# Kernel tuning notes

Measured on AMD Instinct MI355X. Metric: run time of the kernel, lower is better.

## Reference

```python
import jax, jax.numpy as jnp
import numpy as np

N = 50000        # nodes
E = 800000       # edges (avg degree 16)
B = 128          # graphs in batch
NODE_F, EDGE_F, GLOB_F = 16, 8, 32
H = 64           # hidden_dim
L = 4            # num_layers
C = 9            # threshold classes
NG, GE = 20, 16  # num gate types, gate embedding dim
MSG_IN = H + EDGE_F + GE   # 88
UPD_IN = 2 * H             # 128


def _ln(x, g, b):
    mu = x.mean(-1, keepdims=True)
    v = ((x - mu) ** 2).mean(-1, keepdims=True)
    return (x - mu) / jnp.sqrt(v + 1e-5) * g + b


def setup_inputs() -> dict:
    key = jax.random.key(0)
    ks = jax.random.split(key, 24)
    w = lambda k, shp: (jax.random.normal(k, shp, jnp.float32) * 0.05)
    inp = {
        'x': jax.random.normal(ks[0], (N, NODE_F), jnp.float32),
        'edge_index': jax.random.randint(ks[1], (2, E), 0, N, jnp.int32),
        'edge_attr': jax.random.normal(ks[2], (E, EDGE_F), jnp.float32),
        'edge_gate_type': jax.random.randint(ks[3], (E,), 0, NG, jnp.int32),
        'batch': jnp.sort(jax.random.randint(ks[4], (N,), 0, B, jnp.int32)),
        'global_features': jax.random.normal(ks[5], (B, GLOB_F), jnp.float32),
        # node_embed
        'W_embed': w(ks[6], (NODE_F, H)), 'b_embed': jnp.zeros((H,), jnp.float32),
        'g_eln': jnp.ones((H,), jnp.float32), 'b_eln': jnp.zeros((H,), jnp.float32),
        # message-passing layers (stacked over L)
        'mp_gate_emb': w(ks[7], (L, NG, GE)),
        'mp_W_msg': w(ks[8], (L, MSG_IN, H)), 'mp_b_msg': jnp.zeros((L, H), jnp.float32),
        'mp_W_upd': w(ks[9], (L, UPD_IN, H)), 'mp_b_upd': jnp.zeros((L, H), jnp.float32),
        # global_proj
        'W_gproj': w(ks[10], (GLOB_F, H)), 'b_gproj': jnp.zeros((H,), jnp.float32),
        'g_gln': jnp.ones((H,), jnp.float32), 'b_gln': jnp.zeros((H,), jnp.float32),
        # combined_mlp
        'W_c1': w(ks[11], (3 * H + H, 2 * H)), 'b_c1': jnp.zeros((2 * H,), jnp.float32),
        'g_cln': jnp.ones((2 * H,), jnp.float32), 'b_cln': jnp.zeros((2 * H,), jnp.float32),
        'W_c2': w(ks[12], (2 * H, H)), 'b_c2': jnp.zeros((H,), jnp.float32),
        # head
        'W_head': w(ks[13], (H, C)), 'b_head': jnp.zeros((C,), jnp.float32),
    }
    return inp


def reference(x, edge_index, edge_attr, edge_gate_type, batch, global_features,
              W_embed, b_embed, g_eln, b_eln,
              mp_gate_emb, mp_W_msg, mp_b_msg, mp_W_upd, mp_b_upd,
              W_gproj, b_gproj, g_gln, b_gln,
              W_c1, b_c1, g_cln, b_cln, W_c2, b_c2, W_head, b_head):
    n_nodes = x.shape[0]
    n_graphs = global_features.shape[0]
    # node embed (dropout = identity in eval)
    h = _ln(jax.nn.relu(x @ W_embed + b_embed), g_eln, b_eln)  # [N,H]
    src, dst = edge_index[0], edge_index[1]
    for l in range(mp_W_msg.shape[0]):
        ge = mp_gate_emb[l][edge_gate_type]                     # [E,GE] gather
        m_in = jnp.concatenate([h[src], edge_attr, ge], axis=-1)  # [E,MSG_IN]
        m = jax.nn.relu(m_in @ mp_W_msg[l] + mp_b_msg[l])          # [E,H]
        agg = jax.ops.segment_sum(m, dst, num_segments=n_nodes)   # [N,H] scatter-add
        h_new = jnp.concatenate([h, agg], axis=-1) @ mp_W_upd[l] + mp_b_upd[l]
        h = h + h_new                                              # residual
    # multi global pooling
    ones = jnp.ones((n_nodes,), h.dtype)
    counts = jax.ops.segment_sum(ones, batch, num_segments=n_graphs)[:, None]
    h_sum = jax.ops.segment_sum(h, batch, num_segments=n_graphs)
    h_mean = h_sum / jnp.maximum(counts, 1.0)
    h_max = jax.ops.segment_max(h, batch, num_segments=n_graphs)
    h_max = jnp.where(counts > 0, h_max, 0.0)
    h_graph = jnp.concatenate([h_mean, h_max, h_sum], axis=-1)   # [B,3H]
    g = _ln(jax.nn.relu(global_features @ W_gproj + b_gproj), g_gln, b_gln)
    c = jnp.concatenate([h_graph, g], axis=-1)                   # [B,4H]
    c = jax.nn.relu(c @ W_c1 + b_c1)
    c = _ln(c, g_cln, b_cln)
    c = jax.nn.relu(c @ W_c2 + b_c2)
    return c @ W_head + b_head                                   # [B,C]
```

## Files before the change

### kernel.cpp

```cpp
#include <hip/hip_runtime.h>

__device__ __forceinline__ int rfl(int v) { return __builtin_amdgcn_readfirstlane(v); }

__device__ __forceinline__ int lower_bound_dev(const int* __restrict__ a, int n, int v) {
  int lo = 0, hi = n;
  while (lo < hi) { int mid = (lo + hi) >> 1; if (a[mid] < v) lo = mid + 1; else hi = mid; }
  return lo;
}

__global__ void count_kernel(const int* __restrict__ dst, int* __restrict__ counts, int E) {
  int e = blockIdx.x * 256 + threadIdx.x;
  if (e < E) atomicAdd(&counts[dst[e]], 1);
}

__global__ __launch_bounds__(256) void scan_phase1(const int* __restrict__ counts,
                                                   int* __restrict__ row_ptr,
                                                   int* __restrict__ blocksums, int n) {
  int tid = threadIdx.x;
  int i0 = blockIdx.x * 1024 + tid * 4;
  int4 c = make_int4(0, 0, 0, 0);
  if (i0 + 3 < n) {
    c = *(const int4*)(counts + i0);
  } else {
    if (i0 + 0 < n) c.x = counts[i0 + 0];
    if (i0 + 1 < n) c.y = counts[i0 + 1];
    if (i0 + 2 < n) c.z = counts[i0 + 2];
    if (i0 + 3 < n) c.w = counts[i0 + 3];
  }
  int s = c.x + c.y + c.z + c.w;
  int lane = tid & 63, wave = tid >> 6;
  int v = s;
  for (int o = 1; o < 64; o <<= 1) { int u = __shfl_up(v, o); if (lane >= o) v += u; }
  __shared__ int wsum[4];
  if (lane == 63) wsum[wave] = v;
  __syncthreads();
  int woff = 0;
  for (int w = 0; w < wave; w++) woff += wsum[w];
  int excl = woff + (v - s);
  if (tid == 255) blocksums[blockIdx.x] = woff + v;
  int p0 = excl, p1 = p0 + c.x, p2 = p1 + c.y, p3 = p2 + c.z;
  if (i0 + 3 < n) {
    *(int4*)(row_ptr + i0) = make_int4(p0, p1, p2, p3);
  } else {
    if (i0 + 0 < n) row_ptr[i0 + 0] = p0;
    if (i0 + 1 < n) row_ptr[i0 + 1] = p1;
    if (i0 + 2 < n) row_ptr[i0 + 2] = p2;
    if (i0 + 3 < n) row_ptr[i0 + 3] = p3;
  }
}

__global__ __launch_bounds__(64) void scan_phase2(int* __restrict__ blocksums, int nb) {
  int carry = 0;
  for (int base = 0; base < nb; base += 64) {
    int i = base + (int)threadIdx.x;
    int v = (i < nb) ? blocksums[i] : 0;
    int inc = v;
    for (int o = 1; o < 64; o <<= 1) { int u = __shfl_up(inc, o); if ((int)threadIdx.x >= o) inc += u; }
    if (i < nb) blocksums[i] = carry + inc - v;
    carry += __shfl(inc, 63);
  }
}

__global__ __launch_bounds__(256) void scan_phase3(int* __restrict__ row_ptr,
                                                   const int* __restrict__ blocksums,
                                                   int* __restrict__ nextp, int n, int E) {
  int i = blockIdx.x * 256 + threadIdx.x;
  if (i < n) {
    int v = row_ptr[i] + blocksums[i >> 10];
    row_ptr[i] = v;
    nextp[i] = v;
  }
  if (i == 0) row_ptr[n] = E;
}

__global__ void scatter_kernel(const int* __restrict__ src, const int* __restrict__ dst,
                               const int* __restrict__ gt, const float* __restrict__ edge_attr,
                               int* __restrict__ nextp, int2* __restrict__ epk,
                               float* __restrict__ eap, int E) {
  int e = blockIdx.x * 256 + threadIdx.x;
  if (e < E) {
    int p = atomicAdd(&nextp[dst[e]], 1);
    epk[p] = make_int2(src[e], gt[e]);
    const float4* s = (const float4*)(edge_attr + (size_t)e * 8);
    float4 a0 = s[0], a1 = s[1];
    float4* d = (float4*)(eap + (size_t)p * 8);
    d[0] = a0; d[1] = a1;
  }
}

__global__ void gew_kernel(const float* __restrict__ gate_emb, const float* __restrict__ W_msg,
                           float* __restrict__ geW, int nrows) {
  int tid = threadIdx.x;
  int lane = tid & 63;
  int row = blockIdx.x * 4 + (tid >> 6);
  if (row >= nrows) return;
  int l = row / 20, t = row % 20;
  const float* ge = gate_emb + ((size_t)l * 20 + t) * 16;
  const float* W3 = W_msg + (size_t)l * 88 * 64 + 72 * 64;
  float acc = 0.f;
#pragma unroll
  for (int k = 0; k < 16; k++) acc = fmaf(ge[k], W3[(size_t)k * 64 + lane], acc);
  geW[(size_t)row * 64 + lane] = acc;
}

__global__ __launch_bounds__(256) void embed_kernel(const float* __restrict__ x,
                                                    const float* __restrict__ W,
                                                    const float* __restrict__ b,
                                                    const float* __restrict__ gamma,
                                                    const float* __restrict__ beta,
                                                    float* __restrict__ h, int n_nodes) {
  __shared__ float Ws[16 * 64];
  int tid = threadIdx.x;
  for (int i = tid; i < 16 * 64; i += 256) Ws[i] = W[i];
  __syncthreads();
  int lane = tid & 63;
  int n = blockIdx.x * 4 + (tid >> 6);
  if (n >= n_nodes) return;
  const float* xr = x + (size_t)n * 16;
  float acc = b[lane];
#pragma unroll
  for (int k = 0; k < 16; k++) acc = fmaf(xr[k], Ws[k * 64 + lane], acc);
  acc = fmaxf(acc, 0.f);
  float s = acc;
  for (int o = 32; o; o >>= 1) s += __shfl_xor(s, o);
  float mu = s * (1.f / 64.f);
  float d = acc - mu;
  float v = d * d;
  for (int o = 32; o; o >>= 1) v += __shfl_xor(v, o);
  float r = rsqrtf(v * (1.f / 64.f) + 1e-5f);
  h[(size_t)n * 64 + lane] = d * r * gamma[lane] + beta[lane];
}

__global__ __launch_bounds__(256) void nodelin_kernel(const float* __restrict__ A,
                                                      const float* __restrict__ W,
                                                      float* __restrict__ C, int n_nodes) {
  __shared__ float As[64 * 64];
  __shared__ float Bs[64 * 64];
  int tid = threadIdx.x;
  int n0 = blockIdx.x * 64;
#pragma unroll
  for (int i = 0; i < 4; i++) {
    int flat = (tid + i * 256) * 4;
    int r = flat >> 6, k = flat & 63;
    float4 f = make_float4(0.f, 0.f, 0.f, 0.f);
    int n = n0 + r;
    if (n < n_nodes) f = *(const float4*)(A + (size_t)n * 64 + k);
    As[(k + 0) * 64 + r] = f.x;
    As[(k + 1) * 64 + r] = f.y;
    As[(k + 2) * 64 + r] = f.z;
    As[(k + 3) * 64 + r] = f.w;
  }
#pragma unroll
  for (int i = 0; i < 4; i++) {
    int flat = (tid + i * 256) * 4;
    *(float4*)&Bs[flat] = *(const float4*)&W[flat];
  }
  __syncthreads();
  int tx = tid & 15, ty = tid >> 4;
  float acc[4][4] = {{0.f}};
#pragma unroll 4
  for (int k = 0; k < 64; k++) {
    float4 a = *(const float4*)&As[k * 64 + ty * 4];
    float4 bb = *(const float4*)&Bs[k * 64 + tx * 4];
    float av[4] = {a.x, a.y, a.z, a.w};
    float bv[4] = {bb.x, bb.y, bb.z, bb.w};
#pragma unroll
    for (int i = 0; i < 4; i++)
#pragma unroll
      for (int j = 0; j < 4; j++) acc[i][j] = fmaf(av[i], bv[j], acc[i][j]);
  }
#pragma unroll
  for (int i = 0; i < 4; i++) {
    int n = n0 + ty * 4 + i;
    if (n < n_nodes) {
      float4 o = make_float4(acc[i][0], acc[i][1], acc[i][2], acc[i][3]);
      *(float4*)&C[(size_t)n * 64 + tx * 4] = o;
    }
  }
}

__global__ __launch_bounds__(256) void edge_kernel(const float* __restrict__ hW,
                                                   const int2* __restrict__ epk,
                                                   const float* __restrict__ eap,
                                                   const int* __restrict__ row_ptr,
                                                   const float* __restrict__ W_msg_l,
                                                   const float* __restrict__ b_msg_l,
                                                   const float* __restrict__ geW_l,
                                                   float* __restrict__ agg, int n_nodes) {
  __shared__ float geWs[20 * 64];
  int tid = threadIdx.x;
  for (int i = tid; i < 20 * 64; i += 256) geWs[i] = geW_l[i];
  __syncthreads();
  int lane = tid & 63;
  int n = blockIdx.x * 4 + (tid >> 6);
  if (n >= n_nodes) return;
  float w2[8];
#pragma unroll
  for (int k = 0; k < 8; k++) w2[k] = W_msg_l[(size_t)(64 + k) * 64 + lane];
  float bm = b_msg_l[lane];
  int beg = rfl(row_ptr[n]);
  int end = rfl(row_ptr[n + 1]);
  float acc = 0.f;
  int idx = beg;
  for (; idx + 4 <= end; idx += 4) {
    int2 p0 = epk[idx + 0], p1 = epk[idx + 1], p2 = epk[idx + 2], p3 = epk[idx + 3];
    int s0 = rfl(p0.x), t0 = rfl(p0.y);
    int s1 = rfl(p1.x), t1 = rfl(p1.y);
    int s2 = rfl(p2.x), t2 = rfl(p2.y);
    int s3 = rfl(p3.x), t3 = rfl(p3.y);
    float g0 = hW[(size_t)s0 * 64 + lane];
    float g1 = hW[(size_t)s1 * 64 + lane];
    float g2 = hW[(size_t)s2 * 64 + lane];
    float g3 = hW[(size_t)s3 * 64 + lane];
    const float4* ep = (const float4*)(eap + (size_t)idx * 8);
    float4 a00 = ep[0], a01 = ep[1], a10 = ep[2], a11 = ep[3];
    float4 a20 = ep[4], a21 = ep[5], a30 = ep[6], a31 = ep[7];
    float v0 = g0 + geWs[t0 * 64 + lane] + bm;
    v0 = fmaf(a00.x, w2[0], v0); v0 = fmaf(a00.y, w2[1], v0);
    v0 = fmaf(a00.z, w2[2], v0); v0 = fmaf(a00.w, w2[3], v0);
    v0 = fmaf(a01.x, w2[4], v0); v0 = fmaf(a01.y, w2[5], v0);
    v0 = fmaf(a01.z, w2[6], v0); v0 = fmaf(a01.w, w2[7], v0);
    float v1 = g1 + geWs[t1 * 64 + lane] + bm;
    v1 = fmaf(a10.x, w2[0], v1); v1 = fmaf(a10.y, w2[1], v1);
    v1 = fmaf(a10.z, w2[2], v1); v1 = fmaf(a10.w, w2[3], v1);
    v1 = fmaf(a11.x, w2[4], v1); v1 = fmaf(a11.y, w2[5], v1);
    v1 = fmaf(a11.z, w2[6], v1); v1 = fmaf(a11.w, w2[7], v1);
    float v2 = g2 + geWs[t2 * 64 + lane] + bm;
    v2 = fmaf(a20.x, w2[0], v2); v2 = fmaf(a20.y, w2[1], v2);
    v2 = fmaf(a20.z, w2[2], v2); v2 = fmaf(a20.w, w2[3], v2);
    v2 = fmaf(a21.x, w2[4], v2); v2 = fmaf(a21.y, w2[5], v2);
    v2 = fmaf(a21.z, w2[6], v2); v2 = fmaf(a21.w, w2[7], v2);
    float v3 = g3 + geWs[t3 * 64 + lane] + bm;
    v3 = fmaf(a30.x, w2[0], v3); v3 = fmaf(a30.y, w2[1], v3);
    v3 = fmaf(a30.z, w2[2], v3); v3 = fmaf(a30.w, w2[3], v3);
    v3 = fmaf(a31.x, w2[4], v3); v3 = fmaf(a31.y, w2[5], v3);
    v3 = fmaf(a31.z, w2[6], v3); v3 = fmaf(a31.w, w2[7], v3);
    acc += fmaxf(v0, 0.f) + fmaxf(v1, 0.f) + fmaxf(v2, 0.f) + fmaxf(v3, 0.f);
  }
  for (; idx < end; idx++) {
    int2 p = epk[idx];
    int s = rfl(p.x), t = rfl(p.y);
    float g = hW[(size_t)s * 64 + lane];
    const float4* ep = (const float4*)(eap + (size_t)idx * 8);
    float4 a0 = ep[0], a1 = ep[1];
    float v = g + geWs[t * 64 + lane] + bm;
    v = fmaf(a0.x, w2[0], v); v = fmaf(a0.y, w2[1], v);
    v = fmaf(a0.z, w2[2], v); v = fmaf(a0.w, w2[3], v);
    v = fmaf(a1.x, w2[4], v); v = fmaf(a1.y, w2[5], v);
    v = fmaf(a1.z, w2[6], v); v = fmaf(a1.w, w2[7], v);
    acc += fmaxf(v, 0.f);
  }
  agg[(size_t)n * 64 + lane] = acc;
}

__global__ __launch_bounds__(256) void update_fused_kernel(const float* __restrict__ h,
                                                           const float* __restrict__ agg,
                                                           const float* __restrict__ Wu,
                                                           const float* __restrict__ bu,
                                                           const float* __restrict__ W1next,
                                                           float* __restrict__ h_out,
                                                           float* __restrict__ hW_out,
                                                           int n_nodes) {
  __shared__ float As[128 * 64];
  __shared__ float Bs[128 * 64];
  int tid = threadIdx.x;
  int n0 = blockIdx.x * 64;
#pragma unroll
  for (int i = 0; i < 8; i++) {
    int flat = (tid + i * 256) * 4;
    int r = flat >> 7, k = flat & 127;
    float4 f = make_float4(0.f, 0.f, 0.f, 0.f);
    int n = n0 + r;
    if (n < n_nodes) {
      const float* sp = (k < 64) ? (h + (size_t)n * 64 + k) : (agg + (size_t)n * 64 + (k - 64));
      f = *(const float4*)sp;
    }
    As[(k + 0) * 64 + r] = f.x;
    As[(k + 1) * 64 + r] = f.y;
    As[(k + 2) * 64 + r] = f.z;
    As[(k + 3) * 64 + r] = f.w;
  }
#pragma unroll
  for (int i = 0; i < 8; i++) {
    int flat = (tid + i * 256) * 4;
    *(float4*)&Bs[flat] = *(const float4*)&Wu[flat];
  }
  __syncthreads();
  int tx = tid & 15, ty = tid >> 4;
  float acc[4][4] = {{0.f}};
#pragma unroll 4
  for (int k = 0; k < 128; k++) {
    float4 a = *(const float4*)&As[k * 64 + ty * 4];
    float4 bb = *(const float4*)&Bs[k * 64 + tx * 4];
    float av[4] = {a.x, a.y, a.z, a.w};
    float bv[4] = {bb.x, bb.y, bb.z, bb.w};
#pragma unroll
    for (int i = 0; i < 4; i++)
#pragma unroll
      for (int j = 0; j < 4; j++) acc[i][j] = fmaf(av[i], bv[j], acc[i][j]);
  }
  float hnew[4][4];
  float4 bv4 = *(const float4*)&bu[tx * 4];
#pragma unroll
  for (int i = 0; i < 4; i++) {
    int n = n0 + ty * 4 + i;
    if (n < n_nodes) {
      float4 hv = *(const float4*)&h[(size_t)n * 64 + tx * 4];
      hnew[i][0] = hv.x + acc[i][0] + bv4.x;
      hnew[i][1] = hv.y + acc[i][1] + bv4.y;
      hnew[i][2] = hv.z + acc[i][2] + bv4.z;
      hnew[i][3] = hv.w + acc[i][3] + bv4.w;
      float4 o = make_float4(hnew[i][0], hnew[i][1], hnew[i][2], hnew[i][3]);
      *(float4*)&h_out[(size_t)n * 64 + tx * 4] = o;
    } else {
      hnew[i][0] = hnew[i][1] = hnew[i][2] = hnew[i][3] = 0.f;
    }
  }
  if (W1next) {
    __syncthreads();
#pragma unroll
    for (int i = 0; i < 4; i++)
#pragma unroll
      for (int j = 0; j < 4; j++) As[(tx * 4 + j) * 64 + (ty * 4 + i)] = hnew[i][j];
#pragma unroll
    for (int i = 0; i < 4; i++) {
      int flat = (tid + i * 256) * 4;
      *(float4*)&Bs[flat] = *(const float4*)&W1next[flat];
    }
    __syncthreads();
    float acc2[4][4] = {{0.f}};
#pragma unroll 4
    for (int k = 0; k < 64; k++) {
      float4 a = *(const float4*)&As[k * 64 + ty * 4];
      float4 bb = *(const float4*)&Bs[k * 64 + tx * 4];
      float av[4] = {a.x, a.y, a.z, a.w};
      float bv[4] = {bb.x, bb.y, bb.z, bb.w};
#pragma unroll
      for (int i = 0; i < 4; i++)
#pragma unroll
        for (int j = 0; j < 4; j++) acc2[i][j] = fmaf(av[i], bv[j], acc2[i][j]);
    }
#pragma unroll
    for (int i = 0; i < 4; i++) {
      int n = n0 + ty * 4 + i;
      if (n < n_nodes) {
        float4 o = make_float4(acc2[i][0], acc2[i][1], acc2[i][2], acc2[i][3]);
        *(float4*)&hW_out[(size_t)n * 64 + tx * 4] = o;
      }
    }
  }
}

__global__ __launch_bounds__(256) void pool_kernel(const float* __restrict__ h,
                                                   const int* __restrict__ batch,
                                                   float* __restrict__ pooled, int n_nodes) {
  int b = blockIdx.x;
  __shared__ int se[2];
  if (threadIdx.x == 0) se[0] = lower_bound_dev(batch, n_nodes, b);
  if (threadIdx.x == 1) se[1] = lower_bound_dev(batch, n_nodes, b + 1);
  __syncthreads();
  int start = se[0], end = se[1];
  int lane = threadIdx.x & 63, wave = threadIdx.x >> 6;
  float s = 0.f, m = -INFINITY;
  for (int i = start + wave; i < end; i += 4) {
    float v = h[(size_t)i * 64 + lane];
    s += v;
    m = fmaxf(m, v);
  }
  __shared__ float ss[4][64], mm[4][64];
  ss[wave][lane] = s;
  mm[wave][lane] = m;
  __syncthreads();
  if (wave == 0) {
    s = ss[0][lane] + ss[1][lane] + ss[2][lane] + ss[3][lane];
    m = fmaxf(fmaxf(mm[0][lane], mm[1][lane]), fmaxf(mm[2][lane], mm[3][lane]));
    int cnt = end - start;
    float mean = (cnt > 0) ? s / (float)cnt : 0.f;
    if (cnt == 0) { m = 0.f; s = 0.f; }
    pooled[(size_t)b * 192 + lane] = mean;
    pooled[(size_t)b * 192 + 64 + lane] = m;
    pooled[(size_t)b * 192 + 128 + lane] = s;
  }
}

__global__ __launch_bounds__(128) void mlp_kernel(
    const float* __restrict__ pooled, const float* __restrict__ glob,
    const float* __restrict__ W_gproj, const float* __restrict__ b_gproj,
    const float* __restrict__ g_gln, const float* __restrict__ b_gln,
    const float* __restrict__ W_c1, const float* __restrict__ b_c1,
    const float* __restrict__ g_cln, const float* __restrict__ b_cln,
    const float* __restrict__ W_c2, const float* __restrict__ b_c2,
    const float* __restrict__ W_head, const float* __restrict__ b_head,
    float* __restrict__ out) {
  int b = blockIdx.x;
  int tid = threadIdx.x;
  __shared__ float c[256];
  __shared__ float c1s[128];
  __shared__ float c2s[64];
  __shared__ float sred[2][2];
  c[tid] = pooled[(size_t)b * 192 + tid];
  if (tid < 64) c[128 + tid] = pooled[(size_t)b * 192 + 128 + tid];
  if (tid < 64) {
    const float* gf = glob + (size_t)b * 32;
    float acc = b_gproj[tid];
#pragma unroll
    for (int k = 0; k < 32; k++) acc = fmaf(gf[k], W_gproj[(size_t)k * 64 + tid], acc);
    acc = fmaxf(acc, 0.f);
    float s = acc;
    for (int o = 32; o; o >>= 1) s += __shfl_xor(s, o);
    float mu = s * (1.f / 64.f);
    float d = acc - mu;
    float v = d * d;
    for (int o = 32; o; o >>= 1) v += __shfl_xor(v, o);
    float r = rsqrtf(v * (1.f / 64.f) + 1e-5f);
    c[192 + tid] = d * r * g_gln[tid] + b_gln[tid];
  }
  __syncthreads();
  float acc = b_c1[tid];
  for (int k = 0; k < 256; k++) acc = fmaf(c[k], W_c1[(size_t)k * 128 + tid], acc);
  acc = fmaxf(acc, 0.f);
  float s = acc;
  for (int o = 32; o; o >>= 1) s += __shfl_xor(s, o);
  if ((tid & 63) == 0) sred[0][tid >> 6] = s;
  __syncthreads();
  float mu = (sred[0][0] + sred[0][1]) * (1.f / 128.f);
  float d = acc - mu;
  float v = d * d;
  for (int o = 32; o; o >>= 1) v += __shfl_xor(v, o);
  if ((tid & 63) == 0) sred[1][tid >> 6] = v;
  __syncthreads();
  float var = (sred[1][0] + sred[1][1]) * (1.f / 128.f);
  c1s[tid] = d * rsqrtf(var + 1e-5f) * g_cln[tid] + b_cln[tid];
  __syncthreads();
  if (tid < 64) {
    float a2 = b_c2[tid];
    for (int k = 0; k < 128; k++) a2 = fmaf(c1s[k], W_c2[(size_t)k * 64 + tid], a2);
    c2s[tid] = fmaxf(a2, 0.f);
  }
  __syncthreads();
  if (tid < 9) {
    float a3 = b_head[tid];
#pragma unroll
    for (int k = 0; k < 64; k++) a3 = fmaf(c2s[k], W_head[(size_t)k * 9 + tid], a3);
    out[(size_t)b * 9 + tid] = a3;
  }
}

extern "C" void kernel_launch(void* const* d_in, const int* in_sizes, int n_in,
                              void* d_out, int out_size, void* d_ws, size_t ws_size,
                              hipStream_t stream) {
  const float* x       = (const float*)d_in[0];
  const int* edge_index= (const int*)d_in[1];
  const float* edge_attr=(const float*)d_in[2];
  const int* gtype     = (const int*)d_in[3];
  const int* batch     = (const int*)d_in[4];
  const float* glob    = (const float*)d_in[5];
  const float* W_embed = (const float*)d_in[6];
  const float* b_embed = (const float*)d_in[7];
  const float* g_eln   = (const float*)d_in[8];
  const float* b_eln   = (const float*)d_in[9];
  const float* gate_emb= (const float*)d_in[10];
  const float* W_msg   = (const float*)d_in[11];
  const float* b_msg   = (const float*)d_in[12];
  const float* W_upd   = (const float*)d_in[13];
  const float* b_upd   = (const float*)d_in[14];
  const float* W_gproj = (const float*)d_in[15];
  const float* b_gproj = (const float*)d_in[16];
  const float* g_gln   = (const float*)d_in[17];
  const float* b_gln   = (const float*)d_in[18];
  const float* W_c1    = (const float*)d_in[19];
  const float* b_c1    = (const float*)d_in[20];
  const float* g_cln   = (const float*)d_in[21];
  const float* b_cln   = (const float*)d_in[22];
  const float* W_c2    = (const float*)d_in[23];
  const float* b_c2    = (const float*)d_in[24];
  const float* W_head  = (const float*)d_in[25];
  const float* b_head  = (const float*)d_in[26];

  const int N = in_sizes[0] / 16;
  const int E = in_sizes[1] / 2;
  const int B = in_sizes[5] / 32;
  const int L = in_sizes[12] / 64;

  const int* src = edge_index;
  const int* dst = edge_index + E;

  char* ws = (char*)d_ws;
  size_t off = 0;
  auto alloc = [&](size_t bytes) -> void* {
    void* p = ws + off;
    off += (bytes + 255) & ~(size_t)255;
    return p;
  };
  float* h      = (float*)alloc((size_t)N * 64 * 4);
  float* hW     = (float*)alloc((size_t)N * 64 * 4);
  float* agg    = (float*)alloc((size_t)N * 64 * 4);
  float* geW    = (float*)alloc((size_t)L * 20 * 64 * 4);
  float* pooled = (float*)alloc((size_t)B * 192 * 4);
  int* counts   = (int*)alloc((size_t)N * 4);
  int* row_ptr  = (int*)alloc((size_t)(N + 1) * 4);
  int* nextp    = (int*)alloc((size_t)N * 4);
  int nb = (N + 1023) / 1024;
  int* blocksums= (int*)alloc((size_t)nb * 4);
  int2* epk     = (int2*)alloc((size_t)E * 8);
  float* eap    = (float*)alloc((size_t)E * 8 * 4);

  hipMemsetAsync(counts, 0, (size_t)N * 4, stream);
  count_kernel<<<(E + 255) / 256, 256, 0, stream>>>(dst, counts, E);
  scan_phase1<<<nb, 256, 0, stream>>>(counts, row_ptr, blocksums, N);
  scan_phase2<<<1, 64, 0, stream>>>(blocksums, nb);
  scan_phase3<<<(N + 255) / 256, 256, 0, stream>>>(row_ptr, blocksums, nextp, N, E);
  scatter_kernel<<<(E + 255) / 256, 256, 0, stream>>>(src, dst, gtype, edge_attr,
                                                      nextp, epk, eap, E);
  gew_kernel<<<(L * 20 + 3) / 4, 256, 0, stream>>>(gate_emb, W_msg, geW, L * 20);
  embed_kernel<<<(N + 3) / 4, 256, 0, stream>>>(x, W_embed, b_embed, g_eln, b_eln, h, N);

  nodelin_kernel<<<(N + 63) / 64, 256, 0, stream>>>(h, W_msg, hW, N);
  for (int l = 0; l < L; l++) {
    edge_kernel<<<(N + 3) / 4, 256, 0, stream>>>(hW, epk, eap, row_ptr,
                                                 W_msg + (size_t)l * 88 * 64, b_msg + (size_t)l * 64,
                                                 geW + (size_t)l * 20 * 64, agg, N);
    const float* W1next = (l + 1 < L) ? (W_msg + (size_t)(l + 1) * 88 * 64) : nullptr;
    update_fused_kernel<<<(N + 63) / 64, 256, 0, stream>>>(h, agg, W_upd + (size_t)l * 128 * 64,
                                                           b_upd + (size_t)l * 64, W1next, h, hW, N);
  }

  pool_kernel<<<B, 256, 0, stream>>>(h, batch, pooled, N);
  mlp_kernel<<<B, 128, 0, stream>>>(pooled, glob, W_gproj, b_gproj, g_gln, b_gln,
                                    W_c1, b_c1, g_cln, b_cln, W_c2, b_c2,
                                    W_head, b_head, (float*)d_out);
}
```

Measured before the change: 517.4 us.

## Split CSR scatter into permutation plus gather, pack edge metadata, drop LDS staging

Edge sorting now runs in two steps. The first scatters only a permutation index via atomics, and the second gathers src, gate type and edge attributes with coalesced writes. Source and gate type are packed into one 32-bit word (20-bit src), which halves per-edge metadata reads in the edge kernel. The edge kernel also stops staging the gate-weight table in shared memory and reads it directly from global/L2, removing a block-wide barrier. Costs are an extra kernel launch and permutation buffer, plus an implicit limit of fewer than about one million nodes and at most 2047 gate types.

Result: no change. 516.2 us (-0.2%).

```diff
diff --git a/kernel.cpp b/kernel.cpp
--- a/kernel.cpp
+++ b/kernel.cpp
@@ -73,17 +73,22 @@
   if (i == 0) row_ptr[n] = E;
 }
 
-__global__ void scatter_kernel(const int* __restrict__ src, const int* __restrict__ dst,
-                               const int* __restrict__ gt, const float* __restrict__ edge_attr,
-                               int* __restrict__ nextp, int2* __restrict__ epk,
-                               float* __restrict__ eap, int E) {
+__global__ void scatter_perm(const int* __restrict__ dst, int* __restrict__ nextp,
+                             int* __restrict__ perm, int E) {
   int e = blockIdx.x * 256 + threadIdx.x;
-  if (e < E) {
-    int p = atomicAdd(&nextp[dst[e]], 1);
-    epk[p] = make_int2(src[e], gt[e]);
+  if (e < E) { int p = atomicAdd(&nextp[dst[e]], 1); perm[p] = e; }
+}
+
+__global__ void gather_build(const int* __restrict__ perm, const int* __restrict__ src,
+                             const int* __restrict__ gt, const float* __restrict__ edge_attr,
+                             int* __restrict__ epack, float* __restrict__ eap, int E) {
+  int idx = blockIdx.x * 256 + threadIdx.x;
+  if (idx < E) {
+    int e = perm[idx];
+    epack[idx] = (gt[e] << 20) | src[e];
     const float4* s = (const float4*)(edge_attr + (size_t)e * 8);
     float4 a0 = s[0], a1 = s[1];
-    float4* d = (float4*)(eap + (size_t)p * 8);
+    float4* d = (float4*)(eap + (size_t)idx * 8);
     d[0] = a0; d[1] = a1;
   }
 }
@@ -180,17 +185,14 @@
 }
 
 __global__ __launch_bounds__(256) void edge_kernel(const float* __restrict__ hW,
-                                                   const int2* __restrict__ epk,
+                                                   const int* __restrict__ epack,
                                                    const float* __restrict__ eap,
                                                    const int* __restrict__ row_ptr,
                                                    const float* __restrict__ W_msg_l,
                                                    const float* __restrict__ b_msg_l,
                                                    const float* __restrict__ geW_l,
                                                    float* __restrict__ agg, int n_nodes) {
-  __shared__ float geWs[20 * 64];
-  int tid = threadIdx.x;
-  for (int i = tid; i < 20 * 64; i += 256) geWs[i] = geW_l[i];
-  __syncthreads();
+  int tid = threadIdx.x;
   int lane = tid & 63;
   int n = blockIdx.x * 4 + (tid >> 6);
   if (n >= n_nodes) return;
@@ -203,34 +205,41 @@
   float acc = 0.f;
   int idx = beg;
   for (; idx + 4 <= end; idx += 4) {
-    int2 p0 = epk[idx + 0], p1 = epk[idx + 1], p2 = epk[idx + 2], p3 = epk[idx + 3];
-    int s0 = rfl(p0.x), t0 = rfl(p0.y);
-    int s1 = rfl(p1.x), t1 = rfl(p1.y);
-    int s2 = rfl(p2.x), t2 = rfl(p2.y);
-    int s3 = rfl(p3.x), t3 = rfl(p3.y);
+    int p0 = rfl(epack[idx + 0]);
+    int p1 = rfl(epack[idx + 1]);
+    int p2 = rfl(epack[idx + 2]);
+    int p3 = rfl(epack[idx + 3]);
+    int s0 = p0 & 0xFFFFF, t0 = p0 >> 20;
+    int s1 = p1 & 0xFFFFF, t1 = p1 >> 20;
+    int s2 = p2 & 0xFFFFF, t2 = p2 >> 20;
+    int s3 = p3 & 0xFFFFF, t3 = p3 >> 20;
+    const float4* ep = (const float4*)(eap + (size_t)idx * 8);
+    float4 a00 = ep[0], a01 = ep[1], a10 = ep[2], a11 = ep[3];
+    float4 a20 = ep[4], a21 = ep[5], a30 = ep[6], a31 = ep[7];
     float g0 = hW[(size_t)s0 * 64 + lane];
     float g1 = hW[(size_t)s1 * 64 + lane];
     float g2 = hW[(size_t)s2 * 64 + lane];
     float g3 = hW[(size_t)s3 * 64 + lane];
-    const float4* ep = (const float4*)(eap + (size_t)idx * 8);
-    float4 a00 = ep[0], a01 = ep[1], a10 = ep[2], a11 = ep[3];
-    float4 a20 = ep[4], a21 = ep[5], a30 = ep[6], a31 = ep[7];
-    float v0 = g0 + geWs[t0 * 64 + lane] + bm;
+    float e0 = geW_l[t0 * 64 + lane];
+    float e1 = geW_l[t1 * 64 + lane];
+    float e2 = geW_l[t2 * 64 + lane];
+    float e3 = geW_l[t3 * 64 + lane];
+    float v0 = g0 + e0 + bm;
     v0 = fmaf(a00.x, w2[0], v0); v0 = fmaf(a00.y, w2[1], v0);
     v0 = fmaf(a00.z, w2[2], v0); v0 = fmaf(a00.w, w2[3], v0);
     v0 = fmaf(a01.x, w2[4], v0); v0 = fmaf(a01.y, w2[5], v0);
     v0 = fmaf(a01.z, w2[6], v0); v0 = fmaf(a01.w, w2[7], v0);
-    float v1 = g1 + geWs[t1 * 64 + lane] + bm;
+    float v1 = g1 + e1 + bm;
     v1 = fmaf(a10.x, w2[0], v1); v1 = fmaf(a10.y, w2[1], v1);
     v1 = fmaf(a10.z, w2[2], v1); v1 = fmaf(a10.w, w2[3], v1);
     v1 = fmaf(a11.x, w2[4], v1); v1 = fmaf(a11.y, w2[5], v1);
     v1 = fmaf(a11.z, w2[6], v1); v1 = fmaf(a11.w, w2[7], v1);
-    float v2 = g2 + geWs[t2 * 64 + lane] + bm;
+    float v2 = g2 + e2 + bm;
     v2 = fmaf(a20.x, w2[0], v2); v2 = fmaf(a20.y, w2[1], v2);
     v2 = fmaf(a20.z, w2[2], v2); v2 = fmaf(a20.w, w2[3], v2);
     v2 = fmaf(a21.x, w2[4], v2); v2 = fmaf(a21.y, w2[5], v2);
     v2 = fmaf(a21.z, w2[6], v2); v2 = fmaf(a21.w, w2[7], v2);
-    float v3 = g3 + geWs[t3 * 64 + lane] + bm;
+    float v3 = g3 + e3 + bm;
     v3 = fmaf(a30.x, w2[0], v3); v3 = fmaf(a30.y, w2[1], v3);
     v3 = fmaf(a30.z, w2[2], v3); v3 = fmaf(a30.w, w2[3], v3);
     v3 = fmaf(a31.x, w2[4], v3); v3 = fmaf(a31.y, w2[5], v3);
@@ -238,12 +247,12 @@
     acc += fmaxf(v0, 0.f) + fmaxf(v1, 0.f) + fmaxf(v2, 0.f) + fmaxf(v3, 0.f);
   }
   for (; idx < end; idx++) {
-    int2 p = epk[idx];
-    int s = rfl(p.x), t = rfl(p.y);
-    float g = hW[(size_t)s * 64 + lane];
+    int p = rfl(epack[idx]);
+    int s = p & 0xFFFFF, t = p >> 20;
     const float4* ep = (const float4*)(eap + (size_t)idx * 8);
     float4 a0 = ep[0], a1 = ep[1];
-    float v = g + geWs[t * 64 + lane] + bm;
+    float g = hW[(size_t)s * 64 + lane];
+    float v = g + geW_l[t * 64 + lane] + bm;
     v = fmaf(a0.x, w2[0], v); v = fmaf(a0.y, w2[1], v);
     v = fmaf(a0.z, w2[2], v); v = fmaf(a0.w, w2[3], v);
     v = fmaf(a1.x, w2[4], v); v = fmaf(a1.y, w2[5], v);
@@ -502,7 +511,8 @@
   int* nextp    = (int*)alloc((size_t)N * 4);
   int nb = (N + 1023) / 1024;
   int* blocksums= (int*)alloc((size_t)nb * 4);
-  int2* epk     = (int2*)alloc((size_t)E * 8);
+  int* perm     = (int*)alloc((size_t)E * 4);
+  int* epack    = (int*)alloc((size_t)E * 4);
   float* eap    = (float*)alloc((size_t)E * 8 * 4);
 
   hipMemsetAsync(counts, 0, (size_t)N * 4, stream);
@@ -510,14 +520,15 @@
   scan_phase1<<<nb, 256, 0, stream>>>(counts, row_ptr, blocksums, N);
   scan_phase2<<<1, 64, 0, stream>>>(blocksums, nb);
   scan_phase3<<<(N + 255) / 256, 256, 0, stream>>>(row_ptr, blocksums, nextp, N, E);
-  scatter_kernel<<<(E + 255) / 256, 256, 0, stream>>>(src, dst, gtype, edge_attr,
-                                                      nextp, epk, eap, E);
+  scatter_perm<<<(E + 255) / 256, 256, 0, stream>>>(dst, nextp, perm, E);
+  gather_build<<<(E + 255) / 256, 256, 0, stream>>>(perm, src, gtype, edge_attr,
+                                                    epack, eap, E);
   gew_kernel<<<(L * 20 + 3) / 4, 256, 0, stream>>>(gate_emb, W_msg, geW, L * 20);
   embed_kernel<<<(N + 3) / 4, 256, 0, stream>>>(x, W_embed, b_embed, g_eln, b_eln, h, N);
 
   nodelin_kernel<<<(N + 63) / 64, 256, 0, stream>>>(h, W_msg, hW, N);
   for (int l = 0; l < L; l++) {
-    edge_kernel<<<(N + 3) / 4, 256, 0, stream>>>(hW, epk, eap, row_ptr,
+    edge_kernel<<<(N + 3) / 4, 256, 0, stream>>>(hW, epack, eap, row_ptr,
                                                  W_msg + (size_t)l * 88 * 64, b_msg + (size_t)l * 64,
                                                  geW + (size_t)l * 20 * 64, agg, N);
     const float* W1next = (l + 1 < L) ? (W_msg + (size_t)(l + 1) * 88 * 64) : nullptr;
```
